# Kernel optimization log

Measured on AMD Instinct MI355X. Metric: run time of the kernel, lower is better.

Reference implementation:

```python
import jax, jax.numpy as jnp
import numpy as np


def setup_inputs() -> dict:
    key = jax.random.key(0)
    k_y, k_cb = jax.random.split(key)
    B, C, H, W = 8, 192, 64, 64
    G, K = 8, 512
    d = C // G  # 24
    y = jax.random.normal(k_y, (B, C, H, W), dtype=jnp.float32)
    codebooks = jax.random.normal(k_cb, (G, K, d), dtype=jnp.float32)
    return {"y": y, "codebooks": codebooks}


def reference(y, codebooks):
    # y: [B, C, H, W]; codebooks: [G, K, d] with C == G*d
    B, C, H, W = y.shape
    G, K, d = codebooks.shape
    # split channels into G groups of dim d -> vectors at each spatial pos
    x = y.reshape(B, G, d, H, W).transpose(0, 3, 4, 1, 2)  # [B,H,W,G,d]
    x2 = jnp.sum(x * x, axis=-1, keepdims=True)            # [B,H,W,G,1]
    e2 = jnp.sum(codebooks * codebooks, axis=-1)           # [G,K]
    xe = jnp.einsum('bhwgd,gkd->bhwgk', x, codebooks)      # [B,H,W,G,K]
    dist = x2 - 2.0 * xe + e2                              # [B,H,W,G,K]
    idx = jnp.argmin(dist, axis=-1)                        # [B,H,W,G] int
    # gather quantized vectors per group (to_feather)
    q = codebooks[jnp.arange(G), idx]                      # [B,H,W,G,d]
    y_ba = q.transpose(0, 3, 4, 1, 2).reshape(B, C, H, W)  # [B,C,H,W]
    code_index = idx.transpose(0, 3, 1, 2)                 # [B,G,H,W]
    # straight-through estimator
    universal_ctx = y + jax.lax.stop_gradient(y_ba - y)
    return universal_ctx, y_ba, code_index[:, None]        # [B,1,G,H,W]
```

## Files before the change

### kernel.cpp

```cpp
#include <hip/hip_runtime.h>

#define B_   8
#define C_   192
#define HW_  4096
#define G_   8
#define K_   512
#define D_   24
#define CBSZ (K_ * D_)
#define THREADS 256
#define TILES_PER_BLOCK 16

typedef float  f32x4 __attribute__((ext_vector_type(4)));
typedef int    i32x4 __attribute__((ext_vector_type(4)));
typedef short  s16x8 __attribute__((ext_vector_type(8)));
typedef short  s16x4 __attribute__((ext_vector_type(4)));
typedef unsigned long long u64;

static __device__ __forceinline__ unsigned umin_(unsigned a, unsigned b){return a<b?a:b;}
static __device__ __forceinline__ unsigned umax_(unsigned a, unsigned b){return a>b?a:b;}
static __device__ __forceinline__ unsigned short f2bf(float x){
    unsigned u=__float_as_uint(x);
    return (unsigned short)((u + 0x7FFFu + ((u>>16)&1u))>>16);
}
static __device__ __forceinline__ float bf2f(unsigned short h){return __uint_as_float(((unsigned)h)<<16);}

__global__ __launch_bounds__(THREADS, 4) void vq_mfma4(
    const float* __restrict__ y, const float* __restrict__ cb, float* __restrict__ out)
{
    __shared__ unsigned short sB[32 * 512];

    const int bid = blockIdx.x;
    const int g = bid & 7;
    const int chunk = bid >> 3;
    const int tid = threadIdx.x;
    const int wave = tid >> 6, lane = tid & 63;
    const int c = lane & 15, q = lane >> 4;

    const float* cbg = cb + g * CBSZ;

    {
        const f32x4* cb4 = (const f32x4*)cbg;
        for (int i = tid; i < CBSZ/4; i += THREADS) {
            f32x4 v = cb4[i];
            int i4 = i << 2;
            int n  = i4 / 24;
            int k0 = i4 - n * 24;
            int off = (n >> 4) * 512 + (((k0 >> 3) << 4) + (n & 15)) * 8 + (k0 & 7);
            s16x4 h;
            h[0]=(short)f2bf(v[0]); h[1]=(short)f2bf(v[1]);
            h[2]=(short)f2bf(v[2]); h[3]=(short)f2bf(v[3]);
            *(s16x4*)(&sB[off]) = h;
        }
        for (int n = tid; n < K_; n += THREADS) {
            const float* row = cbg + n * D_;
            double s0 = 0.0, s1 = 0.0;
            #pragma unroll
            for (int j = 0; j < D_; j += 2) {
                double v0 = (double)row[j], v1 = (double)row[j+1];
                s0 = fma(v0,v0,s0); s1 = fma(v1,v1,s1);
            }
            double s = s0 + s1;
            unsigned short ehi = f2bf((float)s);
            unsigned short elo = f2bf((float)(s - (double)bf2f(ehi)));
            unsigned* dst = (unsigned*)(&sB[(n >> 4) * 512 + (48 + (n & 15)) * 8]);
            dst[0] = (unsigned)ehi | ((unsigned)elo << 16);
            dst[1] = 0u; dst[2] = 0u; dst[3] = 0u;
        }
    }
    __syncthreads();

    float* out0 = out;
    float* out1 = out + B_*C_*HW_;
    float* out2 = out + 2*B_*C_*HW_;

    for (int mt = wave; mt < TILES_PER_BLOCK; mt += 4) {
        const int posT = chunk * (TILES_PER_BLOCK*16) + mt * 16;
        const int bimg = posT >> 12;
        const int hw   = posT & (HW_-1);
        const int ybase = (bimg*C_ + g*D_)*HW_ + hw;
        const float* yb = y + ybase;

        float xf[8];
        unsigned hx[4], lx[4];
        if (q < 3) {
            const float* yq = yb + (q*8)*HW_ + c;
            #pragma unroll
            for (int jj = 0; jj < 8; ++jj) xf[jj] = -2.0f * yq[jj*HW_];
            #pragma unroll
            for (int p2 = 0; p2 < 4; ++p2) {
                float f0 = xf[2*p2], f1 = xf[2*p2+1];
                unsigned u0 = __float_as_uint(f0), u1v = __float_as_uint(f1);
                hx[p2] = (u1v & 0xFFFF0000u) | (u0 >> 16);
                float l0 = f0 - __uint_as_float(u0 & 0xFFFF0000u);
                float l1 = f1 - __uint_as_float(u1v & 0xFFFF0000u);
                lx[p2] = (unsigned)f2bf(l0) | ((unsigned)f2bf(l1) << 16);
            }
        } else {
            #pragma unroll
            for (int jj = 0; jj < 8; ++jj) xf[jj] = 0.0f;
            hx[0] = 0x3F803F80u; hx[1]=0u; hx[2]=0u; hx[3]=0u;
            lx[0]=0u; lx[1]=0u; lx[2]=0u; lx[3]=0u;
        }
        const s16x8 Xh = __builtin_bit_cast(s16x8, (i32x4){(int)hx[0],(int)hx[1],(int)hx[2],(int)hx[3]});
        const s16x8 Xl = __builtin_bit_cast(s16x8, (i32x4){(int)lx[0],(int)lx[1],(int)lx[2],(int)lx[3]});

        unsigned b1=0xFFFFFFFFu, b2=0xFFFFFFFFu, b3=0xFFFFFFFFu;
        const unsigned qr4 = (unsigned)(q << 2);
        #pragma unroll 8
        for (int t = 0; t < 32; ++t) {
            s16x8 eh = *(const s16x8*)(&sB[t*512 + lane*8]);
            f32x4 acc = {256.0f, 256.0f, 256.0f, 256.0f};
            acc = __builtin_amdgcn_mfma_f32_16x16x32_bf16(eh, Xh, acc, 0,0,0);
            acc = __builtin_amdgcn_mfma_f32_16x16x32_bf16(eh, Xl, acc, 0,0,0);
            const unsigned cbase = ((unsigned)t << 4) + qr4;
            #pragma unroll
            for (int r = 0; r < 4; ++r) {
                unsigned key = (__float_as_uint(acc[r]) & 0xFFFFFE00u) + (cbase + r);
                b3 = umin_(umax_(b2, key), b3);
                b2 = umin_(umax_(b1, key), b2);
                b1 = umin_(b1, key);
            }
        }

        #pragma unroll
        for (int d = 16; d < 64; d <<= 1) {
            unsigned o1=__shfl_xor(b1,d,64), o2=__shfl_xor(b2,d,64), o3=__shfl_xor(b3,d,64);
            unsigned x = umax_(b1,o1);
            unsigned yv= umin_(b2,o2);
            unsigned w = umax_(b2,o2);
            unsigned z = umin_(b3,o3);
            b1 = umin_(b1,o1);
            b2 = umin_(x,yv);
            b3 = umin_(umax_(x,yv), umin_(w,z));
        }

        const float v1 = __uint_as_float(b1 & 0xFFFFFE00u);
        const float v2 = __uint_as_float(b2 & 0xFFFFFE00u);
        int kwin;
        if (__ballot((v2 - v1) < 0.20f) == 0ull) {
            kwin = (int)(b1 & 511u);
        } else {
            double xd[8];
            #pragma unroll
            for (int jj = 0; jj < 8; ++jj) xd[jj] = (double)xf[jj];
            const unsigned cands[3] = {b1, b2, b3};
            u64 bestk = ~0ull;
            #pragma unroll
            for (int ci = 0; ci < 3; ++ci) {
                int kc = (int)(cands[ci] & 511u);
                double s = 0.0;
                if (q < 3) {
                    const f32x4* ce4 = (const f32x4*)(cbg + kc*D_ + (q<<3));
                    float ef[8];
                    *(f32x4*)&ef[0] = ce4[0];
                    *(f32x4*)&ef[4] = ce4[1];
                    #pragma unroll
                    for (int jj = 0; jj < 8; ++jj) {
                        double ev = (double)ef[jj];
                        s = fma(ev, ev, s);
                        s = fma(xd[jj], ev, s);
                    }
                }
                s += __shfl_xor(s, 16, 64);
                s += __shfl_xor(s, 32, 64);
                s += 256.0;
                u64 kk = (((u64)__double_as_longlong(s)) & ~0x1FFull) | (u64)kc;
                bestk = kk < bestk ? kk : bestk;
            }
            kwin = (int)(bestk & 511ull);
        }

        const float* cw = cbg + kwin * D_;
        if (q < 3) {
            const f32x4* cw4 = (const f32x4*)(cw + (q<<3));
            float v[8];
            *(f32x4*)&v[0] = cw4[0];
            *(f32x4*)&v[4] = cw4[1];
            const int ob = ybase + (q*8)*HW_ + c;
            #pragma unroll
            for (int jj = 0; jj < 8; ++jj) {
                out0[ob + jj*HW_] = v[jj];
                out1[ob + jj*HW_] = v[jj];
            }
        }
        if (lane < 16)
            out2[(bimg*G_ + g)*HW_ + hw + lane] = (float)kwin;
    }
}

extern "C" void kernel_launch(void* const* d_in, const int* in_sizes, int n_in,
                              void* d_out, int out_size, void* d_ws, size_t ws_size,
                              hipStream_t stream) {
    const float* y  = (const float*)d_in[0];
    const float* cb = (const float*)d_in[1];
    float* out = (float*)d_out;

    const int nblocks = 128 * G_;
    vq_mfma4<<<dim3(nblocks), dim3(THREADS), 0, stream>>>(y, cb, out);
}
```

Baseline: 119.5 us.

## Precompute bf16 codebook image in a staging kernel and copy it into LDS

Adds a small pre-kernel that converts each group's codebook to the bf16 MFMA-ready layout, with norm hi/lo terms, once into workspace. The main kernel then fills its shared memory with a plain 16-byte vector copy instead of converting and computing double-precision norms in every block. Tiles per block are halved, doubling the block count, and launch bounds now request 5 blocks per CU. The cost is an extra kernel launch and workspace traffic, and each block still copies 32 KB into LDS to process fewer tiles.

```diff
diff --git a/kernel.cpp b/kernel.cpp
--- a/kernel.cpp
+++ b/kernel.cpp
@@ -8,7 +8,7 @@
 #define D_   24
 #define CBSZ (K_ * D_)
 #define THREADS 256
-#define TILES_PER_BLOCK 16
+#define TILES_PER_BLOCK 8
 
 typedef float  f32x4 __attribute__((ext_vector_type(4)));
 typedef int    i32x4 __attribute__((ext_vector_type(4)));
@@ -24,8 +24,47 @@
 }
 static __device__ __forceinline__ float bf2f(unsigned short h){return __uint_as_float(((unsigned)h)<<16);}
 
-__global__ __launch_bounds__(THREADS, 4) void vq_mfma4(
-    const float* __restrict__ y, const float* __restrict__ cb, float* __restrict__ out)
+__global__ __launch_bounds__(THREADS) void vq_stage(
+    const float* __restrict__ cb, unsigned short* __restrict__ ws)
+{
+    const int g = blockIdx.x >> 3;
+    const int s = blockIdx.x & 7;
+    const int tid = threadIdx.x;
+    const float* cbg = cb + g * CBSZ;
+    unsigned short* img = ws + g * 16384;
+
+    for (int i = tid; i < 384; i += THREADS) {
+        int gi = s * 384 + i;
+        f32x4 v = ((const f32x4*)cbg)[gi];
+        int i4 = gi << 2;
+        int n  = i4 / 24;
+        int k0 = i4 - n * 24;
+        int off = (n >> 4) * 512 + (((k0 >> 3) << 4) + (n & 15)) * 8 + (k0 & 7);
+        s16x4 h;
+        h[0]=(short)f2bf(v[0]); h[1]=(short)f2bf(v[1]);
+        h[2]=(short)f2bf(v[2]); h[3]=(short)f2bf(v[3]);
+        *(s16x4*)(&img[off]) = h;
+    }
+    if (tid < 64) {
+        int n = s * 64 + tid;
+        const float* row = cbg + n * D_;
+        double s0 = 0.0, s1 = 0.0;
+        #pragma unroll
+        for (int j = 0; j < D_; j += 2) {
+            double v0 = (double)row[j], v1 = (double)row[j+1];
+            s0 = fma(v0,v0,s0); s1 = fma(v1,v1,s1);
+        }
+        double sv = s0 + s1;
+        unsigned short ehi = f2bf((float)sv);
+        unsigned short elo = f2bf((float)(sv - (double)bf2f(ehi)));
+        i32x4 pack = { (int)((unsigned)ehi | ((unsigned)elo << 16)), 0, 0, 0 };
+        *(i32x4*)(&img[(n >> 4) * 512 + (48 + (n & 15)) * 8]) = pack;
+    }
+}
+
+__global__ __launch_bounds__(THREADS, 5) void vq_mfma5(
+    const float* __restrict__ y, const float* __restrict__ cb,
+    const unsigned short* __restrict__ ws, float* __restrict__ out)
 {
     __shared__ unsigned short sB[32 * 512];
 
@@ -39,33 +78,11 @@
     const float* cbg = cb + g * CBSZ;
 
     {
-        const f32x4* cb4 = (const f32x4*)cbg;
-        for (int i = tid; i < CBSZ/4; i += THREADS) {
-            f32x4 v = cb4[i];
-            int i4 = i << 2;
-            int n  = i4 / 24;
-            int k0 = i4 - n * 24;
-            int off = (n >> 4) * 512 + (((k0 >> 3) << 4) + (n & 15)) * 8 + (k0 & 7);
-            s16x4 h;
-            h[0]=(short)f2bf(v[0]); h[1]=(short)f2bf(v[1]);
-            h[2]=(short)f2bf(v[2]); h[3]=(short)f2bf(v[3]);
-            *(s16x4*)(&sB[off]) = h;
-        }
-        for (int n = tid; n < K_; n += THREADS) {
-            const float* row = cbg + n * D_;
-            double s0 = 0.0, s1 = 0.0;
-            #pragma unroll
-            for (int j = 0; j < D_; j += 2) {
-                double v0 = (double)row[j], v1 = (double)row[j+1];
-                s0 = fma(v0,v0,s0); s1 = fma(v1,v1,s1);
-            }
-            double s = s0 + s1;
-            unsigned short ehi = f2bf((float)s);
-            unsigned short elo = f2bf((float)(s - (double)bf2f(ehi)));
-            unsigned* dst = (unsigned*)(&sB[(n >> 4) * 512 + (48 + (n & 15)) * 8]);
-            dst[0] = (unsigned)ehi | ((unsigned)elo << 16);
-            dst[1] = 0u; dst[2] = 0u; dst[3] = 0u;
-        }
+        const char* src = (const char*)(ws + g * 16384);
+        char* dst = (char*)sB;
+        #pragma unroll
+        for (int it = 0; it < 8; ++it)
+            *(i32x4*)(dst + it*4096 + tid*16) = *(const i32x4*)(src + it*4096 + tid*16);
     }
     __syncthreads();
 
@@ -194,7 +211,9 @@
     const float* y  = (const float*)d_in[0];
     const float* cb = (const float*)d_in[1];
     float* out = (float*)d_out;
-
-    const int nblocks = 128 * G_;
-    vq_mfma4<<<dim3(nblocks), dim3(THREADS), 0, stream>>>(y, cb, out);
-}
+    unsigned short* ws = (unsigned short*)d_ws;
+
+    vq_stage<<<dim3(64), dim3(THREADS), 0, stream>>>(cb, ws);
+    const int nblocks = 256 * G_;
+    vq_mfma5<<<dim3(nblocks), dim3(THREADS), 0, stream>>>(y, cb, ws, out);
+}
```

Measured after the change: 117.7 us. About the same (-1.5%).
